# Kernel optimization log

Measured on AMD Instinct MI355X. Metric: run time of the kernel, lower is better.

## Reference

```python
import jax, jax.numpy as jnp
import numpy as np

N_QUBITS = 8
N_CYCLES = 4
B = 8192
C64 = jnp.complex64

# ---- gate matrices ----

def _ry_batched(t):  # t: [B] -> [B,2,2]
    c = jnp.cos(t / 2).astype(C64)
    s = jnp.sin(t / 2).astype(C64)
    return jnp.stack([jnp.stack([c, -s], -1), jnp.stack([s, c], -1)], -2)


def _rz_batched(p):  # p: [B] -> [B,2,2]
    e0 = jnp.exp(-0.5j * p.astype(C64))
    e1 = jnp.exp(0.5j * p.astype(C64))
    z = jnp.zeros_like(e0)
    return jnp.stack([jnp.stack([e0, z], -1), jnp.stack([z, e1], -1)], -2)


def _rx(t):  # scalar -> [2,2]
    c = jnp.cos(t / 2).astype(C64)
    s = (-1j * jnp.sin(t / 2)).astype(C64)
    return jnp.stack([jnp.stack([c, s]), jnp.stack([s, c])])


def _crx(t):  # scalar -> [4,4] block-diag(I2, RX(t)), control = first index
    return jnp.eye(4, dtype=C64).at[2:, 2:].set(_rx(t))


def _u3(t, p, l):  # scalars -> [2,2]
    ct = jnp.cos(t / 2).astype(C64)
    st = jnp.sin(t / 2).astype(C64)
    eil = jnp.exp(1j * l.astype(C64))
    eip = jnp.exp(1j * p.astype(C64))
    return jnp.stack([jnp.stack([ct, -eil * st]), jnp.stack([eip * st, eip * eil * ct])])

CNOT = jnp.array([[1, 0, 0, 0], [0, 1, 0, 0], [0, 0, 0, 1], [0, 0, 1, 0]], dtype=C64)

# ---- statevector ops (state: [B] + [2]*N_QUBITS) ----

def apply_1q(state, U, wire):
    b = state.shape[0]
    s = jnp.moveaxis(state, 1 + wire, 1).reshape(b, 2, -1)
    s = jnp.einsum('bij,bjk->bik', U, s) if U.ndim == 3 else jnp.einsum('ij,bjk->bik', U, s)
    return jnp.moveaxis(s.reshape((b,) + (2,) * N_QUBITS), 1, 1 + wire)


def apply_2q(state, U, wc, wt):
    b = state.shape[0]
    s = jnp.moveaxis(state, (1 + wc, 1 + wt), (1, 2)).reshape(b, 4, -1)
    s = jnp.einsum('ij,bjk->bik', U, s)
    return jnp.moveaxis(s.reshape((b,) + (2,) * N_QUBITS), (1, 2), (1 + wc, 1 + wt))


def expval_z(state, wire):  # <Z_wire> : [B]
    probs = state.real ** 2 + state.imag ** 2
    axes = tuple(a for a in range(1, N_QUBITS + 1) if a != 1 + wire)
    z = jnp.sum(probs, axis=axes)  # [B,2]
    return z[:, 0] - z[:, 1]


def _circuit(theta, phi, crx_params, u3_params):
    b = theta.shape[0]
    state = jnp.zeros((b, 2 ** N_QUBITS), dtype=C64).at[:, 0].set(1.0)
    state = state.reshape((b,) + (2,) * N_QUBITS)
    # circuit builder: RY(theta), RZ(phi) on every wire + CNOT ring, n_cycles times
    U = jnp.einsum('bij,bjk->bik', _rz_batched(phi), _ry_batched(theta))  # RZ @ RY, [B,2,2]
    for _ in range(N_CYCLES):
        for w in range(N_QUBITS):
            state = apply_1q(state, U, w)
        for w in range(N_QUBITS):
            state = apply_2q(state, CNOT, w, (w + 1) % N_QUBITS)
    # QCNN layer 1
    for i, (c, t) in enumerate([(0, 1), (2, 3), (4, 5), (6, 7), (1, 2), (3, 4), (5, 6)]):
        state = apply_2q(state, _crx(crx_params[i]), c, t)
    # (intermediate expvals on [0,2,4,6] are computed then discarded in original)
    for i, w in enumerate([1, 3, 5, 7]):
        p = u3_params[i]
        state = apply_1q(state, _u3(p[0], p[1], p[2]), w)
    for i, (c, t) in enumerate([(1, 3), (5, 7), (3, 5)]):
        state = apply_2q(state, _crx(crx_params[7 + i]), c, t)
    for i, w in enumerate([3, 7]):
        p = u3_params[4 + i]
        state = apply_1q(state, _u3(p[0], p[1], p[2]), w)
    state = apply_2q(state, _crx(crx_params[10]), 3, 7)
    p = u3_params[6]
    state = apply_1q(state, _u3(p[0], p[1], p[2]), 7)
    ev = expval_z(state, 7)[:, None]  # [B,1]
    return jax.nn.relu(ev)


def setup_inputs() -> dict:
    key = jax.random.key(0)
    k1, k2, k3, k4 = jax.random.split(key, 4)
    two_pi = 2.0 * np.pi
    return {
        'theta': jax.random.uniform(k1, (B,), jnp.float32, 0.0, two_pi),
        'phi': jax.random.uniform(k2, (B,), jnp.float32, 0.0, two_pi),
        'crx_params': jax.random.uniform(k3, (11,), jnp.float32, 0.0, two_pi),
        'u3_params': jax.random.uniform(k4, (7, 3), jnp.float32, 0.0, two_pi),
    }


def reference(theta, phi, crx_params, u3_params):
    return _circuit(theta, phi, crx_params, u3_params)
```

## Files before the change

kernel.cpp:

```cpp
#include <hip/hip_runtime.h>
#include <math.h>


typedef float v2f __attribute__((ext_vector_type(2)));

__device__ __forceinline__ v2f pkmul(v2f a, v2f b) {
  v2f d; asm("v_pk_mul_f32 %0, %1, %2" : "=v"(d) : "v"(a), "v"(b)); return d;
}
__device__ __forceinline__ v2f pkfma(v2f a, v2f b, v2f c) {
  v2f d; asm("v_pk_fma_f32 %0, %1, %2, %3" : "=v"(d) : "v"(a), "v"(b), "v"(c)); return d;
}
__device__ __forceinline__ v2f dup(float x) { return (v2f){x, x}; }

template <int M>
__device__ __forceinline__ float shxm(float v) {
  if constexpr (M == 1 || M == 2 || M == 3 || M == 7 || M == 8 || M == 15) {
    constexpr int ctrl = (M == 1) ? 0xB1 : (M == 2) ? 0x4E : (M == 3) ? 0x1B
                         : (M == 7) ? 0x141 : (M == 8) ? 0x128 : 0x140;
    return __int_as_float(__builtin_amdgcn_update_dpp(
        0, __float_as_int(v), ctrl, 0xF, 0xF, true));
  } else {
    return __shfl_xor(v, M, 64);
  }
}
template <int M>
__device__ __forceinline__ v2f shf2(v2f a) {
  return (v2f){shxm<M>(a.x), shxm<M>(a.y)};
}

struct G1 { float r00, i00, r01, i01, r10, i10, r11, i11; };

__device__ __forceinline__ void cplx_fma(v2f& R, v2f& I, v2f PR, v2f PI,
                                         v2f cAr, v2f cAi, v2f cAiN,
                                         v2f cBr, v2f cBi, v2f cBiN) {
  v2f NR = pkfma(cBiN, PI, pkfma(cBr, PR, pkfma(cAiN, I, pkmul(cAr, R))));
  v2f NI = pkfma(cBi, PR, pkfma(cBr, PI, pkfma(cAi, R, pkmul(cAr, I))));
  R = NR; I = NI;
}

__device__ __forceinline__ void apply_pair(v2f& LR, v2f& LI, v2f& HR, v2f& HI,
                                           float g00r, float g00i, float g01r,
                                           float g01i, float g10r, float g10i,
                                           float g11r, float g11i) {
  const v2f a00r = dup(g00r), a00i = dup(g00i), n00i = dup(-g00i);
  const v2f a01r = dup(g01r), a01i = dup(g01i), n01i = dup(-g01i);
  const v2f a10r = dup(g10r), a10i = dup(g10i), n10i = dup(-g10i);
  const v2f a11r = dup(g11r), a11i = dup(g11i), n11i = dup(-g11i);
  v2f NLR = pkfma(n01i, HI, pkfma(a01r, HR, pkfma(n00i, LI, pkmul(a00r, LR))));
  v2f NLI = pkfma(a01i, HR, pkfma(a01r, HI, pkfma(a00i, LR, pkmul(a00r, LI))));
  v2f NHR = pkfma(n11i, HI, pkfma(a11r, HR, pkfma(n10i, LI, pkmul(a10r, LR))));
  v2f NHI = pkfma(a11i, HR, pkfma(a11r, HI, pkfma(a10i, LR, pkmul(a10r, LI))));
  LR = NLR; LI = NLI; HR = NHR; HI = NHI;
}

__device__ __forceinline__ void crx_pairv(v2f& LR, v2f& LI, v2f& HR, v2f& HI,
                                          v2f cCC, v2f cSS, v2f cSSN) {
  v2f NLR = pkfma(cSS, HI, pkmul(cCC, LR));
  v2f NLI = pkfma(cSSN, HR, pkmul(cCC, LI));
  v2f NHR = pkfma(cSS, LI, pkmul(cCC, HR));
  v2f NHI = pkfma(cSSN, LR, pkmul(cCC, HI));
  LR = NLR; LI = NLI; HR = NHR; HI = NHI;
}

template <int RL, int VL>
__device__ __forceinline__ void u_lane(v2f (&CR)[4], v2f (&CI)[4], int l,
                                       float uAr, float uBi, float uAip,
                                       float uBrp) {
  const bool hi = (__popc(l & RL) & 1) != 0;
  const float Ai = hi ? uAip : -uAip;
  const float Br = hi ? uBrp : -uBrp;
  const v2f cAr = dup(uAr), cAi = dup(Ai), cAiN = dup(-Ai);
  const v2f cBr = dup(Br), cBi = dup(uBi), cBiN = dup(-uBi);
  v2f PR[4], PI[4];
#pragma unroll
  for (int q = 0; q < 4; ++q) { PR[q] = shf2<VL>(CR[q]); PI[q] = shf2<VL>(CI[q]); }
#pragma unroll
  for (int q = 0; q < 4; ++q)
    cplx_fma(CR[q], CI[q], PR[q], PI[q], cAr, cAi, cAiN, cBr, cBi, cBiN);
}

__device__ __forceinline__ void u_reg4(v2f (&CR)[4], v2f (&CI)[4], float uAr,
                                       float uBi, float uAip, float uBrp) {
#pragma unroll
  for (int q = 0; q < 4; ++q) {
    const float lr = CR[q].x, li = CI[q].x, hr = CR[q].y, hj = CI[q].y;
    CR[q] = (v2f){uAr * lr + uAip * li - uBrp * hr - uBi * hj,
                  uBrp * lr - uBi * li + uAr * hr - uAip * hj};
    CI[q] = (v2f){uAr * li - uAip * lr - uBrp * hj + uBi * hr,
                  uBrp * li + uBi * lr + uAr * hj + uAip * hr};
  }
}

template <int RL>
__device__ __forceinline__ void cnot_lr4(v2f (&CR)[4], v2f (&CI)[4], int l) {
  const bool c = (__popc(l & RL) & 1) != 0;
#pragma unroll
  for (int q = 0; q < 4; ++q) {
    const float ax = CR[q].x, ay = CR[q].y;
    CR[q] = (v2f){c ? ay : ax, c ? ax : ay};
    const float bx = CI[q].x, by = CI[q].y;
    CI[q] = (v2f){c ? by : bx, c ? bx : by};
  }
}

__device__ __forceinline__ void cnot_swap42(v2f (&CR)[4], v2f (&CI)[4]) {
  float t;
  t = CR[0].y; CR[0].y = CR[2].y; CR[2].y = t;
  t = CR[1].y; CR[1].y = CR[3].y; CR[3].y = t;
  t = CI[0].y; CI[0].y = CI[2].y; CI[2].y = t;
  t = CI[1].y; CI[1].y = CI[3].y; CI[3].y = t;
}

__device__ __forceinline__ void cnot_swap21(v2f (&CR)[4], v2f (&CI)[4]) {
  v2f t;
  t = CR[2]; CR[2] = CR[3]; CR[3] = t;
  t = CI[2]; CI[2] = CI[3]; CI[3] = t;
}

template <int VL>
__device__ __forceinline__ void cnot_rl(v2f (&CR)[4], v2f (&CI)[4]) {
  CR[1] = shf2<VL>(CR[1]); CI[1] = shf2<VL>(CI[1]);
  CR[3] = shf2<VL>(CR[3]); CI[3] = shf2<VL>(CI[3]);
}

template <int RL, int VL>
__device__ __forceinline__ void crx_ll(v2f (&CR)[4], v2f (&CI)[4], int l,
                                       float co, float si) {
  const bool c = (__popc(l & RL) & 1) != 0;
  const float cc = c ? co : 1.f, ss = c ? si : 0.f;
  const v2f cCC = dup(cc), cSS = dup(ss), cSSN = dup(-ss);
  v2f PR[4], PI[4];
#pragma unroll
  for (int q = 0; q < 4; ++q) { PR[q] = shf2<VL>(CR[q]); PI[q] = shf2<VL>(CI[q]); }
#pragma unroll
  for (int q = 0; q < 4; ++q) {
    CR[q] = pkfma(cSS, PI[q], pkmul(cCC, CR[q]));
    CI[q] = pkfma(cSSN, PR[q], pkmul(cCC, CI[q]));
  }
}

template <int RL>
__device__ __forceinline__ void crx_lr4(v2f (&CR)[4], v2f (&CI)[4], int l,
                                        float co, float si) {
  const bool c = (__popc(l & RL) & 1) != 0;
  const float cc = c ? co : 1.f, ss = c ? si : 0.f;
#pragma unroll
  for (int q = 0; q < 4; ++q) {
    const float rx = CR[q].x, ry = CR[q].y, ix = CI[q].x, iy = CI[q].y;
    CR[q] = (v2f){cc * rx + ss * iy, cc * ry + ss * ix};
    CI[q] = (v2f){cc * ix - ss * ry, cc * iy - ss * rx};
  }
}

template <int RL, int VL>
__device__ __forceinline__ void u3_lane(v2f (&CR)[4], v2f (&CI)[4], int l,
                                        const G1& g) {
  const bool hi = (__popc(l & RL) & 1) != 0;
  const float Ar = hi ? g.r11 : g.r00, Aii = hi ? g.i11 : g.i00;
  const float Br = hi ? g.r10 : g.r01, Bi = hi ? g.i10 : g.i01;
  const v2f cAr = dup(Ar), cAi = dup(Aii), cAiN = dup(-Aii);
  const v2f cBr = dup(Br), cBi = dup(Bi), cBiN = dup(-Bi);
  v2f PR[4], PI[4];
#pragma unroll
  for (int q = 0; q < 4; ++q) { PR[q] = shf2<VL>(CR[q]); PI[q] = shf2<VL>(CI[q]); }
#pragma unroll
  for (int q = 0; q < 4; ++q)
    cplx_fma(CR[q], CI[q], PR[q], PI[q], cAr, cAi, cAiN, cBr, cBi, cBiN);
}

__device__ __forceinline__ void u3_reg4(v2f (&CR)[4], v2f (&CI)[4], const G1& g) {
#pragma unroll
  for (int q = 0; q < 4; ++q) {
    const float lr = CR[q].x, li = CI[q].x, hr = CR[q].y, hj = CI[q].y;
    CR[q] = (v2f){g.r00 * lr - g.i00 * li + g.r01 * hr - g.i01 * hj,
                  g.r10 * lr - g.i10 * li + g.r11 * hr - g.i11 * hj};
    CI[q] = (v2f){g.r00 * li + g.i00 * lr + g.r01 * hj + g.i01 * hr,
                  g.r10 * li + g.i10 * lr + g.r11 * hj + g.i11 * hr};
  }
}

__device__ __forceinline__ G1 u3_gate(const float* __restrict__ u3p, int k) {
  float st, ct, sp, cp, sl, cl;
  __sincosf(0.5f * u3p[3 * k], &st, &ct);
  __sincosf(u3p[3 * k + 1], &sp, &cp);
  __sincosf(u3p[3 * k + 2], &sl, &cl);
  G1 g;
  g.r00 = ct;        g.i00 = 0.f;
  g.r01 = -cl * st;  g.i01 = -sl * st;
  g.r10 = cp * st;   g.i10 = sp * st;
  g.r11 = (cp * cl - sp * sl) * ct;
  g.i11 = (sp * cl + cp * sl) * ct;
  return g;
}

__global__ __launch_bounds__(256, 4) void qcnn_kernel(
    const float* __restrict__ theta, const float* __restrict__ phi,
    const float* __restrict__ crx, const float* __restrict__ u3p,
    float* __restrict__ out, int nbatch) {
  const int tid = blockIdx.x * blockDim.x + threadIdx.x;
  const int wave = tid >> 6;
  const int lane = threadIdx.x & 63;
  const int l = lane & 31;
  int b = wave * 2 + (lane >> 5);
  if (b >= nbatch) b = nbatch - 1;

  v2f CR[4], CI[4];
#pragma unroll
  for (int q = 0; q < 4; ++q) { CR[q] = dup(0.f); CI[q] = dup(0.f); }
  if (l == 0) CR[0].x = 1.f;

  const float th = theta[b], ph = phi[b];
  float sth, cth, sph, cph;
  __sincosf(0.5f * th, &sth, &cth);
  __sincosf(0.5f * ph, &sph, &cph);
  const float uAr = cph * cth, uBi = sph * sth;
  const float uAip = sph * cth, uBrp = cph * sth;

#define ULANE(RL, VL) u_lane<RL, VL>(CR, CI, l, uAr, uBi, uAip, uBrp)
#define UPAIR(a, b_) apply_pair(CR[a], CI[a], CR[b_], CI[b_], uAr, -uAip, \
                                -uBrp, uBi, uBrp, uBi, uAr, uAip)
#define UREGS() do { u_reg4(CR, CI, uAr, uBi, uAip, uBrp); \
                     UPAIR(0, 2); UPAIR(1, 3); \
                     UPAIR(0, 1); UPAIR(2, 3); } while (0)
#define RING(RL45, VL70) do { cnot_lr4<RL45>(CR, CI, l); \
                              cnot_swap42(CR, CI); cnot_swap21(CR, CI); \
                              cnot_rl<VL70>(CR, CI); } while (0)

  ULANE(16, 16); ULANE(8, 8);   ULANE(4, 4);   ULANE(2, 2);  ULANE(1, 1);
  UREGS(); RING(31, 24);
  ULANE(16, 24); ULANE(24, 12); ULANE(28, 6);  ULANE(30, 3); ULANE(31, 1);
  UREGS(); RING(21, 20);
  ULANE(16, 20); ULANE(8, 10);  ULANE(20, 5);  ULANE(10, 2); ULANE(21, 1);
  UREGS(); RING(19, 30);
  ULANE(16, 30); ULANE(24, 15); ULANE(12, 7);  ULANE(6, 3);  ULANE(19, 1);
  UREGS(); RING(17, 17);
#undef RING
#undef UREGS
#undef UPAIR
#undef ULANE

  float co, si;
#define LD(k) __sincosf(0.5f * crx[k], &si, &co)
  LD(0); crx_ll<16, 8>(CR, CI, l, co, si);
  LD(1); crx_ll<4, 2>(CR, CI, l, co, si);
  LD(2); crx_lr4<17>(CR, CI, l, co, si);
  LD(3);
  crx_pairv(CR[2], CI[2], CR[3], CI[3], dup(co), dup(si), dup(-si));
  LD(4); crx_ll<8, 4>(CR, CI, l, co, si);
  LD(5); crx_ll<2, 1>(CR, CI, l, co, si);
  LD(6);
  {
    const v2f cCC = (v2f){1.f, co}, cSS = (v2f){0.f, si}, cSSN = (v2f){0.f, -si};
    crx_pairv(CR[0], CI[0], CR[2], CI[2], cCC, cSS, cSSN);
    crx_pairv(CR[1], CI[1], CR[3], CI[3], cCC, cSS, cSSN);
  }

  { G1 g = u3_gate(u3p, 0); u3_lane<8, 8>(CR, CI, l, g); }
  { G1 g = u3_gate(u3p, 1); u3_lane<2, 2>(CR, CI, l, g); }
  { G1 g = u3_gate(u3p, 2); u3_reg4(CR, CI, g); }
  { G1 g = u3_gate(u3p, 3);
    apply_pair(CR[0], CI[0], CR[1], CI[1], g.r00, g.i00, g.r01, g.i01,
               g.r10, g.i10, g.r11, g.i11);
    apply_pair(CR[2], CI[2], CR[3], CI[3], g.r00, g.i00, g.r01, g.i01,
               g.r10, g.i10, g.r11, g.i11); }

  LD(7); crx_ll<8, 2>(CR, CI, l, co, si);
  LD(8);
  {
    const v2f cCC = (v2f){1.f, co}, cSS = (v2f){0.f, si}, cSSN = (v2f){0.f, -si};
    crx_pairv(CR[0], CI[0], CR[1], CI[1], cCC, cSS, cSSN);
    crx_pairv(CR[2], CI[2], CR[3], CI[3], cCC, cSS, cSSN);
  }
  LD(9); crx_lr4<2>(CR, CI, l, co, si);

  { G1 g = u3_gate(u3p, 4); u3_lane<2, 2>(CR, CI, l, g); }
  { G1 g = u3_gate(u3p, 5);
    apply_pair(CR[0], CI[0], CR[1], CI[1], g.r00, g.i00, g.r01, g.i01,
               g.r10, g.i10, g.r11, g.i11);
    apply_pair(CR[2], CI[2], CR[3], CI[3], g.r00, g.i00, g.r01, g.i01,
               g.r10, g.i10, g.r11, g.i11); }

  LD(10);
  {
    const bool c = (__popc(l & 2) & 1) != 0;
    const float cc = c ? co : 1.f, ss = c ? si : 0.f;
    const v2f cCC = dup(cc), cSS = dup(ss), cSSN = dup(-ss);
    crx_pairv(CR[0], CI[0], CR[1], CI[1], cCC, cSS, cSSN);
    crx_pairv(CR[2], CI[2], CR[3], CI[3], cCC, cSS, cSSN);
  }

  { G1 g = u3_gate(u3p, 6);
    apply_pair(CR[0], CI[0], CR[1], CI[1], g.r00, g.i00, g.r01, g.i01,
               g.r10, g.i10, g.r11, g.i11);
    apply_pair(CR[2], CI[2], CR[3], CI[3], g.r00, g.i00, g.r01, g.i01,
               g.r10, g.i10, g.r11, g.i11); }
#undef LD

  v2f S0 = pkfma(CI[0], CI[0], pkmul(CR[0], CR[0]));
  v2f S1 = pkfma(CI[1], CI[1], pkmul(CR[1], CR[1]));
  v2f S2 = pkfma(CI[2], CI[2], pkmul(CR[2], CR[2]));
  v2f S3 = pkfma(CI[3], CI[3], pkmul(CR[3], CR[3]));
  const v2f T = (S0 + S2) - (S1 + S3);
  float v = T.x + T.y;
  v += shxm<1>(v); v += shxm<2>(v); v += shxm<4>(v);
  v += shxm<8>(v); v += shxm<16>(v);
  if (l == 0) out[b] = fmaxf(v, 0.f);
}

extern "C" void kernel_launch(void* const* d_in, const int* in_sizes, int n_in,
                              void* d_out, int out_size, void* d_ws, size_t ws_size,
                              hipStream_t stream) {
  const float* theta = (const float*)d_in[0];
  const float* phi = (const float*)d_in[1];
  const float* crx = (const float*)d_in[2];
  const float* u3p = (const float*)d_in[3];
  float* out = (float*)d_out;
  const int nb = in_sizes[0];
  const int elems_per_block = 8;
  dim3 block(256);
  dim3 grid((nb + elems_per_block - 1) / elems_per_block);
  qcnn_kernel<<<grid, block, 0, stream>>>(theta, phi, crx, u3p, out, nb);
}
```

Measured before the change: 79.25 us.

## Precompute gate constants in prep kernel, use op_sel packed math and ds_swizzle

Adds a one-block prep kernel that computes the CRX cos/sin pairs and the U3 matrices once into workspace, so the main kernel loads them instead of having every thread run sincos. The register-local gates (u_reg4, u3_reg4, crx_lr4) are rewritten with v_pk_fma/v_pk_mul op_sel variants to keep packed math without unpacking lanes. Non-DPP xor shuffles now use ds_swizzle instead of __shfl_xor. The cost is an extra kernel launch and a dependency on the workspace, and the inline-asm op_sel semantics must be right for the results to stay correct.

New measurement: 78.18 us. No clear change (-1.4%).

```diff
diff --git a/kernel.cpp b/kernel.cpp
--- a/kernel.cpp
+++ b/kernel.cpp
@@ -9,6 +9,22 @@
 }
 __device__ __forceinline__ v2f pkfma(v2f a, v2f b, v2f c) {
   v2f d; asm("v_pk_fma_f32 %0, %1, %2, %3" : "=v"(d) : "v"(a), "v"(b), "v"(c)); return d;
+}
+__device__ __forceinline__ v2f pkmul_lo1(v2f a, v2f b) {
+  v2f d; asm("v_pk_mul_f32 %0, %1, %2 op_sel:[0,0] op_sel_hi:[1,0]"
+             : "=v"(d) : "v"(a), "v"(b)); return d;
+}
+__device__ __forceinline__ v2f pkfma_lo1(v2f a, v2f b, v2f c) {
+  v2f d; asm("v_pk_fma_f32 %0, %1, %2, %3 op_sel:[0,0,0] op_sel_hi:[1,0,1]"
+             : "=v"(d) : "v"(a), "v"(b), "v"(c)); return d;
+}
+__device__ __forceinline__ v2f pkfma_hi1(v2f a, v2f b, v2f c) {
+  v2f d; asm("v_pk_fma_f32 %0, %1, %2, %3 op_sel:[0,1,0] op_sel_hi:[1,1,1]"
+             : "=v"(d) : "v"(a), "v"(b), "v"(c)); return d;
+}
+__device__ __forceinline__ v2f pkfma_sw1(v2f a, v2f b, v2f c) {
+  v2f d; asm("v_pk_fma_f32 %0, %1, %2, %3 op_sel:[0,1,0] op_sel_hi:[1,0,1]"
+             : "=v"(d) : "v"(a), "v"(b), "v"(c)); return d;
 }
 __device__ __forceinline__ v2f dup(float x) { return (v2f){x, x}; }
 
@@ -20,7 +36,8 @@
     return __int_as_float(__builtin_amdgcn_update_dpp(
         0, __float_as_int(v), ctrl, 0xF, 0xF, true));
   } else {
-    return __shfl_xor(v, M, 64);
+    return __int_as_float(__builtin_amdgcn_ds_swizzle(
+        __float_as_int(v), (M << 10) | 0x1F));
   }
 }
 template <int M>
@@ -79,16 +96,38 @@
     cplx_fma(CR[q], CI[q], PR[q], PI[q], cAr, cAi, cAiN, cBr, cBi, cBiN);
 }
 
+__device__ __forceinline__ void gate_pack(v2f (&CR)[4], v2f (&CI)[4],
+                                          v2f cA, v2f cB, v2f cBn,
+                                          v2f cC, v2f cD, v2f cDn) {
+#pragma unroll
+  for (int q = 0; q < 4; ++q) {
+    v2f NR = pkfma_hi1(cDn, CI[q], pkfma_hi1(cC, CR[q],
+             pkfma_lo1(cBn, CI[q], pkmul_lo1(cA, CR[q]))));
+    v2f NI = pkfma_hi1(cD, CR[q], pkfma_hi1(cC, CI[q],
+             pkfma_lo1(cB, CR[q], pkmul_lo1(cA, CI[q]))));
+    CR[q] = NR; CI[q] = NI;
+  }
+}
+
 __device__ __forceinline__ void u_reg4(v2f (&CR)[4], v2f (&CI)[4], float uAr,
                                        float uBi, float uAip, float uBrp) {
-#pragma unroll
-  for (int q = 0; q < 4; ++q) {
-    const float lr = CR[q].x, li = CI[q].x, hr = CR[q].y, hj = CI[q].y;
-    CR[q] = (v2f){uAr * lr + uAip * li - uBrp * hr - uBi * hj,
-                  uBrp * lr - uBi * li + uAr * hr - uAip * hj};
-    CI[q] = (v2f){uAr * li - uAip * lr - uBrp * hj + uBi * hr,
-                  uBrp * li + uBi * lr + uAr * hj + uAip * hr};
-  }
+  gate_pack(CR, CI,
+            (v2f){uAr, uBrp},
+            (v2f){-uAip, uBi},
+            (v2f){uAip, -uBi},
+            (v2f){-uBrp, uAr},
+            (v2f){uBi, uAip},
+            (v2f){-uBi, -uAip});
+}
+
+__device__ __forceinline__ void u3_reg4(v2f (&CR)[4], v2f (&CI)[4], const G1& g) {
+  gate_pack(CR, CI,
+            (v2f){g.r00, g.r10},
+            (v2f){g.i00, g.i10},
+            (v2f){-g.i00, -g.i10},
+            (v2f){g.r01, g.r11},
+            (v2f){g.i01, g.i11},
+            (v2f){-g.i01, -g.i11});
 }
 
 template <int RL>
@@ -144,11 +183,12 @@
                                         float co, float si) {
   const bool c = (__popc(l & RL) & 1) != 0;
   const float cc = c ? co : 1.f, ss = c ? si : 0.f;
+  const v2f cc2 = dup(cc), ss2 = dup(ss), ssN2 = dup(-ss);
 #pragma unroll
   for (int q = 0; q < 4; ++q) {
-    const float rx = CR[q].x, ry = CR[q].y, ix = CI[q].x, iy = CI[q].y;
-    CR[q] = (v2f){cc * rx + ss * iy, cc * ry + ss * ix};
-    CI[q] = (v2f){cc * ix - ss * ry, cc * iy - ss * rx};
+    v2f NR = pkfma_sw1(ss2, CI[q], pkmul(cc2, CR[q]));
+    v2f NI = pkfma_sw1(ssN2, CR[q], pkmul(cc2, CI[q]));
+    CR[q] = NR; CI[q] = NI;
   }
 }
 
@@ -168,35 +208,40 @@
     cplx_fma(CR[q], CI[q], PR[q], PI[q], cAr, cAi, cAiN, cBr, cBi, cBiN);
 }
 
-__device__ __forceinline__ void u3_reg4(v2f (&CR)[4], v2f (&CI)[4], const G1& g) {
-#pragma unroll
-  for (int q = 0; q < 4; ++q) {
-    const float lr = CR[q].x, li = CI[q].x, hr = CR[q].y, hj = CI[q].y;
-    CR[q] = (v2f){g.r00 * lr - g.i00 * li + g.r01 * hr - g.i01 * hj,
-                  g.r10 * lr - g.i10 * li + g.r11 * hr - g.i11 * hj};
-    CI[q] = (v2f){g.r00 * li + g.i00 * lr + g.r01 * hj + g.i01 * hr,
-                  g.r10 * li + g.i10 * lr + g.r11 * hj + g.i11 * hr};
-  }
-}
-
-__device__ __forceinline__ G1 u3_gate(const float* __restrict__ u3p, int k) {
-  float st, ct, sp, cp, sl, cl;
-  __sincosf(0.5f * u3p[3 * k], &st, &ct);
-  __sincosf(u3p[3 * k + 1], &sp, &cp);
-  __sincosf(u3p[3 * k + 2], &sl, &cl);
+__device__ __forceinline__ G1 load_g1(const float* __restrict__ cs, int k) {
+  const float* p = cs + 22 + 8 * k;
   G1 g;
-  g.r00 = ct;        g.i00 = 0.f;
-  g.r01 = -cl * st;  g.i01 = -sl * st;
-  g.r10 = cp * st;   g.i10 = sp * st;
-  g.r11 = (cp * cl - sp * sl) * ct;
-  g.i11 = (sp * cl + cp * sl) * ct;
+  g.r00 = p[0]; g.i00 = p[1]; g.r01 = p[2]; g.i01 = p[3];
+  g.r10 = p[4]; g.i10 = p[5]; g.r11 = p[6]; g.i11 = p[7];
   return g;
+}
+
+__global__ void prep_kernel(const float* __restrict__ crx,
+                            const float* __restrict__ u3p,
+                            float* __restrict__ ws) {
+  const int t = threadIdx.x;
+  if (t < 11) {
+    float s, c;
+    sincosf(0.5f * crx[t], &s, &c);
+    ws[2 * t] = c; ws[2 * t + 1] = s;
+  } else if (t >= 16 && t < 23) {
+    const int k = t - 16;
+    float st, ct, sp, cp, sl, cl;
+    sincosf(0.5f * u3p[3 * k], &st, &ct);
+    sincosf(u3p[3 * k + 1], &sp, &cp);
+    sincosf(u3p[3 * k + 2], &sl, &cl);
+    float* o = ws + 22 + 8 * k;
+    o[0] = ct;            o[1] = 0.f;
+    o[2] = -cl * st;      o[3] = -sl * st;
+    o[4] = cp * st;       o[5] = sp * st;
+    o[6] = (cp * cl - sp * sl) * ct;
+    o[7] = (sp * cl + cp * sl) * ct;
+  }
 }
 
 __global__ __launch_bounds__(256, 4) void qcnn_kernel(
     const float* __restrict__ theta, const float* __restrict__ phi,
-    const float* __restrict__ crx, const float* __restrict__ u3p,
-    float* __restrict__ out, int nbatch) {
+    const float* __restrict__ cs, float* __restrict__ out, int nbatch) {
   const int tid = blockIdx.x * blockDim.x + threadIdx.x;
   const int wave = tid >> 6;
   const int lane = threadIdx.x & 63;
@@ -239,42 +284,41 @@
 #undef UPAIR
 #undef ULANE
 
-  float co, si;
-#define LD(k) __sincosf(0.5f * crx[k], &si, &co)
-  LD(0); crx_ll<16, 8>(CR, CI, l, co, si);
-  LD(1); crx_ll<4, 2>(CR, CI, l, co, si);
-  LD(2); crx_lr4<17>(CR, CI, l, co, si);
+#define LD(k) const float co##k = cs[2 * k], si##k = cs[2 * k + 1]
+  LD(0); crx_ll<16, 8>(CR, CI, l, co0, si0);
+  LD(1); crx_ll<4, 2>(CR, CI, l, co1, si1);
+  LD(2); crx_lr4<17>(CR, CI, l, co2, si2);
   LD(3);
-  crx_pairv(CR[2], CI[2], CR[3], CI[3], dup(co), dup(si), dup(-si));
-  LD(4); crx_ll<8, 4>(CR, CI, l, co, si);
-  LD(5); crx_ll<2, 1>(CR, CI, l, co, si);
+  crx_pairv(CR[2], CI[2], CR[3], CI[3], dup(co3), dup(si3), dup(-si3));
+  LD(4); crx_ll<8, 4>(CR, CI, l, co4, si4);
+  LD(5); crx_ll<2, 1>(CR, CI, l, co5, si5);
   LD(6);
   {
-    const v2f cCC = (v2f){1.f, co}, cSS = (v2f){0.f, si}, cSSN = (v2f){0.f, -si};
+    const v2f cCC = (v2f){1.f, co6}, cSS = (v2f){0.f, si6}, cSSN = (v2f){0.f, -si6};
     crx_pairv(CR[0], CI[0], CR[2], CI[2], cCC, cSS, cSSN);
     crx_pairv(CR[1], CI[1], CR[3], CI[3], cCC, cSS, cSSN);
   }
 
-  { G1 g = u3_gate(u3p, 0); u3_lane<8, 8>(CR, CI, l, g); }
-  { G1 g = u3_gate(u3p, 1); u3_lane<2, 2>(CR, CI, l, g); }
-  { G1 g = u3_gate(u3p, 2); u3_reg4(CR, CI, g); }
-  { G1 g = u3_gate(u3p, 3);
+  { G1 g = load_g1(cs, 0); u3_lane<8, 8>(CR, CI, l, g); }
+  { G1 g = load_g1(cs, 1); u3_lane<2, 2>(CR, CI, l, g); }
+  { G1 g = load_g1(cs, 2); u3_reg4(CR, CI, g); }
+  { G1 g = load_g1(cs, 3);
     apply_pair(CR[0], CI[0], CR[1], CI[1], g.r00, g.i00, g.r01, g.i01,
                g.r10, g.i10, g.r11, g.i11);
     apply_pair(CR[2], CI[2], CR[3], CI[3], g.r00, g.i00, g.r01, g.i01,
                g.r10, g.i10, g.r11, g.i11); }
 
-  LD(7); crx_ll<8, 2>(CR, CI, l, co, si);
+  LD(7); crx_ll<8, 2>(CR, CI, l, co7, si7);
   LD(8);
   {
-    const v2f cCC = (v2f){1.f, co}, cSS = (v2f){0.f, si}, cSSN = (v2f){0.f, -si};
+    const v2f cCC = (v2f){1.f, co8}, cSS = (v2f){0.f, si8}, cSSN = (v2f){0.f, -si8};
     crx_pairv(CR[0], CI[0], CR[1], CI[1], cCC, cSS, cSSN);
     crx_pairv(CR[2], CI[2], CR[3], CI[3], cCC, cSS, cSSN);
   }
-  LD(9); crx_lr4<2>(CR, CI, l, co, si);
-
-  { G1 g = u3_gate(u3p, 4); u3_lane<2, 2>(CR, CI, l, g); }
-  { G1 g = u3_gate(u3p, 5);
+  LD(9); crx_lr4<2>(CR, CI, l, co9, si9);
+
+  { G1 g = load_g1(cs, 4); u3_lane<2, 2>(CR, CI, l, g); }
+  { G1 g = load_g1(cs, 5);
     apply_pair(CR[0], CI[0], CR[1], CI[1], g.r00, g.i00, g.r01, g.i01,
                g.r10, g.i10, g.r11, g.i11);
     apply_pair(CR[2], CI[2], CR[3], CI[3], g.r00, g.i00, g.r01, g.i01,
@@ -283,13 +327,13 @@
   LD(10);
   {
     const bool c = (__popc(l & 2) & 1) != 0;
-    const float cc = c ? co : 1.f, ss = c ? si : 0.f;
+    const float cc = c ? co10 : 1.f, ss = c ? si10 : 0.f;
     const v2f cCC = dup(cc), cSS = dup(ss), cSSN = dup(-ss);
     crx_pairv(CR[0], CI[0], CR[1], CI[1], cCC, cSS, cSSN);
     crx_pairv(CR[2], CI[2], CR[3], CI[3], cCC, cSS, cSSN);
   }
 
-  { G1 g = u3_gate(u3p, 6);
+  { G1 g = load_g1(cs, 6);
     apply_pair(CR[0], CI[0], CR[1], CI[1], g.r00, g.i00, g.r01, g.i01,
                g.r10, g.i10, g.r11, g.i11);
     apply_pair(CR[2], CI[2], CR[3], CI[3], g.r00, g.i00, g.r01, g.i01,
@@ -315,9 +359,13 @@
   const float* crx = (const float*)d_in[2];
   const float* u3p = (const float*)d_in[3];
   float* out = (float*)d_out;
+  float* ws = (float*)d_ws;
   const int nb = in_sizes[0];
+
+  prep_kernel<<<1, 64, 0, stream>>>(crx, u3p, ws);
+
   const int elems_per_block = 8;
   dim3 block(256);
   dim3 grid((nb + elems_per_block - 1) / elems_per_block);
-  qcnn_kernel<<<grid, block, 0, stream>>>(theta, phi, crx, u3p, out, nb);
-}
+  qcnn_kernel<<<grid, block, 0, stream>>>(theta, phi, ws, out, nb);
+}
```
